# Optimization experiments

Hardware: AMD Instinct MI355X
Metric: run time of the kernel (lower is better)

## Reference

```python
import jax, jax.numpy as jnp
import numpy as np

N_NODES = 50000   # number of graph nodes
N_EDGES = 800000  # avg degree 16
D_IN = 128
D_OUT = 128


def setup_inputs() -> dict:
    key = jax.random.key(0)
    k = jax.random.split(key, 5)
    seq = jax.random.normal(k[0], (N_NODES, D_IN), dtype=jnp.float32)
    # Linear weight, torch layout [out_dim, in_dim], xavier-ish scale
    W = jax.random.normal(k[1], (D_OUT, D_IN), dtype=jnp.float32) * (1.414 / np.sqrt(D_IN))
    b = jnp.zeros((D_OUT,), dtype=jnp.float32)  # bias init fill_(0.0)
    # COO sparse adjacency: out[row] += val * seq_proj[col]
    edge_row = jax.random.randint(k[2], (N_EDGES,), 0, N_NODES, dtype=jnp.int32)
    edge_col = jax.random.randint(k[3], (N_EDGES,), 0, N_NODES, dtype=jnp.int32)
    edge_val = jax.random.uniform(k[4], (N_EDGES,), dtype=jnp.float32)
    return {"seq": seq, "W": W, "b": b,
            "edge_row": edge_row, "edge_col": edge_col, "edge_val": edge_val}


def reference(seq, W, b, edge_row, edge_col, edge_val):
    # seq = self.fc(seq): [N, D_in] @ [D_in, D_out]
    h = seq @ W.T                                   # [N, D_out]
    # out = torch.spmm(adj, h): COO gather-scale-scatter
    msgs = h[edge_col] * edge_val[:, None]          # [E, D_out]
    out = jax.ops.segment_sum(msgs, edge_row, num_segments=N_NODES)  # [N, D_out]
    # bias add + relu (fused epilogue)
    return jax.nn.relu(out + b)
```

## Files before the change

### kernel.cpp

```cpp
#include <hip/hip_runtime.h>

#define NN 50000
#define NE 800000
#define DD 128

#define BK_SHIFT 8
#define NBUCK 196
#define CHUNK 2048
#define NCHUNK 391
#define NGB 782
#define ECAP 8192

#define OFF_H      0
#define OFF_EBIN   3200000
#define OFF_EPACK  6411264
#define OFF_END    8016896
#define OFF_CUR    8066896
#define WS_FULL_FLOATS 8067092

typedef short short8 __attribute__((ext_vector_type(8)));
typedef float f32x4 __attribute__((ext_vector_type(4)));

static __device__ __forceinline__ unsigned int f2bf(float x) {
    unsigned int u = __float_as_uint(x);
    return (u + 0x7fffu + ((u >> 16) & 1u)) >> 16;
}

__global__ __launch_bounds__(256) void k1_scatter_gemm(
        const float* __restrict__ seq, const float* __restrict__ W,
        unsigned short* __restrict__ h,
        const int* __restrict__ erow, const int* __restrict__ ecol,
        const float* __restrict__ eval,
        int* __restrict__ gcur, uint2* __restrict__ ebin) {
    __shared__ uint4 lds4[3072];
    char* lds = (char*)lds4;
    const int t = threadIdx.x;

    if (blockIdx.x < NCHUNK) {
        int* lh = (int*)lds4;
        for (int i = t; i < NBUCK; i += 256) lh[i] = 0;
        __syncthreads();
        const int e0 = blockIdx.x * CHUNK;
        for (int i = t; i < CHUNK; i += 256) {
            int e = e0 + i;
            if (e < NE) atomicAdd(&lh[erow[e] >> BK_SHIFT], 1);
        }
        __syncthreads();
        for (int i = t; i < NBUCK; i += 256) {
            int c = lh[i];
            lh[i] = c ? atomicAdd(&gcur[i], c) : 0;
        }
        __syncthreads();
        for (int i = t; i < CHUNK; i += 256) {
            int e = e0 + i;
            if (e < NE) {
                int r = erow[e], c = ecol[e];
                unsigned int vb = __float_as_uint(eval[e]);
                int k = r >> BK_SHIFT;
                int pos = atomicAdd(&lh[k], 1);
                if (pos < ECAP)
                    ebin[(size_t)k * ECAP + pos] =
                        make_uint2(((unsigned)r << 16) | (unsigned)c, vb);
            }
        }
        return;
    }

    const int base = (blockIdx.x - NCHUNK) * 64;
#define BS_OFF 16384

    {
        const int o = t >> 1, ksb = (t & 1) * 64;
        const float4* Wr = (const float4*)(W + o * 128 + ksb);
#pragma unroll
        for (int i = 0; i < 16; i += 2) {
            float4 x = Wr[i], y = Wr[i + 1];
            uint4 p;
            p.x = f2bf(x.x) | (f2bf(x.y) << 16);
            p.y = f2bf(x.z) | (f2bf(x.w) << 16);
            p.z = f2bf(y.x) | (f2bf(y.y) << 16);
            p.w = f2bf(y.z) | (f2bf(y.w) << 16);
            int byte = o * 256 + (ksb + i * 4) * 2;
            *(uint4*)(lds + BS_OFF + (byte ^ ((o & 7) << 4))) = p;
        }
    }
    {
        const int row = t >> 2, n = base + row;
        const int c0 = (t & 3) * 4;
        const float4* Sr = (const float4*)(seq + (size_t)n * 128);
        const bool ok = (n < NN);
#pragma unroll
        for (int i = 0; i < 4; ++i) {
            int cc = c0 + i;
            float4 x = ok ? Sr[cc * 2]     : make_float4(0.f, 0.f, 0.f, 0.f);
            float4 y = ok ? Sr[cc * 2 + 1] : make_float4(0.f, 0.f, 0.f, 0.f);
            uint4 p;
            p.x = f2bf(x.x) | (f2bf(x.y) << 16);
            p.y = f2bf(x.z) | (f2bf(x.w) << 16);
            p.z = f2bf(y.x) | (f2bf(y.y) << 16);
            p.w = f2bf(y.z) | (f2bf(y.w) << 16);
            int byte = row * 256 + cc * 16;
            *(uint4*)(lds + (byte ^ ((row & 7) << 4))) = p;
        }
    }
    __syncthreads();

    const int l = t & 63, wv = t >> 6;
    const int lr = l & 15, kg = l >> 4;
    const int arow = wv * 16 + lr;
    f32x4 acc[8] = {};

#pragma unroll
    for (int ks = 0; ks < 4; ++ks) {
        const int kbyte = ks * 64 + kg * 16;
        short8 av = *(short8*)(lds + ((arow * 256 + kbyte) ^ ((arow & 7) << 4)));
#pragma unroll
        for (int c = 0; c < 8; ++c) {
            const int o = c * 16 + lr;
            short8 bv = *(short8*)(lds + BS_OFF +
                                   ((o * 256 + kbyte) ^ ((o & 7) << 4)));
            acc[c] = __builtin_amdgcn_mfma_f32_16x16x32_bf16(av, bv, acc[c], 0, 0, 0);
        }
    }

#pragma unroll
    for (int c = 0; c < 8; ++c) {
#pragma unroll
        for (int r = 0; r < 4; ++r) {
            int n = base + wv * 16 + kg * 4 + r;
            if (n < NN)
                h[(size_t)n * DD + c * 16 + lr] = (unsigned short)f2bf(acc[c][r]);
        }
    }
}

__global__ __launch_bounds__(256) void csr_fill(const uint2* __restrict__ ebin,
                                                const int* __restrict__ gcur,
                                                int* __restrict__ endv,
                                                unsigned int* __restrict__ epack) {
    __shared__ int lh[256];
    __shared__ int lx[256];
    const int k = blockIdx.x;
    const int t = threadIdx.x;
    const size_t s0 = (size_t)k * ECAP;
    int cnt = gcur[k];
    if (cnt > ECAP) cnt = ECAP;
    const size_t s1 = s0 + cnt;
    const int r0 = k << BK_SHIFT;

    lh[t] = 0;
    __syncthreads();
    for (size_t e = s0 + t; e < s1; e += 256)
        atomicAdd(&lh[(ebin[e].x >> 16) & 255], 1);
    __syncthreads();

    const int myc = lh[t];
    lx[t] = myc;
    __syncthreads();
    for (int off = 1; off < 256; off <<= 1) {
        int y = (t >= off) ? lx[t - off] : 0;
        __syncthreads();
        lx[t] += y;
        __syncthreads();
    }
    const int incl = lx[t];
    const int row = r0 + t;
    if (row < NN) endv[row] = (int)s0 + incl;
    __syncthreads();
    lh[t] = (int)s0 + incl - myc;
    __syncthreads();

    for (size_t e = s0 + t; e < s1; e += 256) {
        uint2 ed = ebin[e];
        int pos = atomicAdd(&lh[(ed.x >> 16) & 255], 1);
        epack[pos] = (ed.x & 0xffffu) | (f2bf(__uint_as_float(ed.y)) << 16);
    }
}

__global__ __launch_bounds__(256) void gather_kernel(const unsigned short* __restrict__ h,
                                                     const int* __restrict__ end,
                                                     const unsigned int* __restrict__ epack,
                                                     const float* __restrict__ b,
                                                     float* __restrict__ out) {
    const int row  = blockIdx.x * 4 + (threadIdx.x >> 6);
    const int lane = threadIdx.x & 63;
    const int slot = lane >> 4;
    const int sub  = lane & 15;
    const int begin = (row & 255) ? end[row - 1] : (row >> BK_SHIFT) * ECAP;
    const int e1 = end[row];

    float acc[8] = {0.f, 0.f, 0.f, 0.f, 0.f, 0.f, 0.f, 0.f};
    const unsigned short* hp = h + sub * 8;

#define BODY(EE) do {                                                          \
        unsigned int cv = __builtin_nontemporal_load(epack + (EE));            \
        float v = __uint_as_float(cv & 0xffff0000u);                           \
        uint4 hv = *(const uint4*)(hp + (size_t)(cv & 0xffffu) * DD);          \
        unsigned int uu;                                                       \
        uu = hv.x;                                                             \
        acc[0] = fmaf(v, __uint_as_float(uu << 16),          acc[0]);          \
        acc[1] = fmaf(v, __uint_as_float(uu & 0xffff0000u),  acc[1]);          \
        uu = hv.y;                                                             \
        acc[2] = fmaf(v, __uint_as_float(uu << 16),          acc[2]);          \
        acc[3] = fmaf(v, __uint_as_float(uu & 0xffff0000u),  acc[3]);          \
        uu = hv.z;                                                             \
        acc[4] = fmaf(v, __uint_as_float(uu << 16),          acc[4]);          \
        acc[5] = fmaf(v, __uint_as_float(uu & 0xffff0000u),  acc[5]);          \
        uu = hv.w;                                                             \
        acc[6] = fmaf(v, __uint_as_float(uu << 16),          acc[6]);          \
        acc[7] = fmaf(v, __uint_as_float(uu & 0xffff0000u),  acc[7]);          \
    } while (0)

    int e = begin + slot;
    for (; e + 12 < e1; e += 16) { BODY(e); BODY(e + 4); BODY(e + 8); BODY(e + 12); }
    for (; e < e1; e += 4) BODY(e);
#undef BODY

#pragma unroll
    for (int i = 0; i < 8; ++i) {
        acc[i] += __shfl_xor(acc[i], 16);
        acc[i] += __shfl_xor(acc[i], 32);
    }

    if (slot == 0) {
        const float4* b4 = (const float4*)(b + sub * 8);
        float4 b0 = b4[0], b1 = b4[1];
        f32x4 o0, o1;
        o0.x = fmaxf(acc[0] + b0.x, 0.f);
        o0.y = fmaxf(acc[1] + b0.y, 0.f);
        o0.z = fmaxf(acc[2] + b0.z, 0.f);
        o0.w = fmaxf(acc[3] + b0.w, 0.f);
        o1.x = fmaxf(acc[4] + b1.x, 0.f);
        o1.y = fmaxf(acc[5] + b1.y, 0.f);
        o1.z = fmaxf(acc[6] + b1.z, 0.f);
        o1.w = fmaxf(acc[7] + b1.w, 0.f);
        f32x4* op = (f32x4*)(out + (size_t)row * DD + sub * 8);
        __builtin_nontemporal_store(o0, op);
        __builtin_nontemporal_store(o1, op + 1);
    }
}

extern "C" void kernel_launch(void* const* d_in, const int* in_sizes, int n_in,
                              void* d_out, int out_size, void* d_ws, size_t ws_size,
                              hipStream_t stream) {
    const float* seq  = (const float*)d_in[0];
    const float* W    = (const float*)d_in[1];
    const float* b    = (const float*)d_in[2];
    const int*   erow = (const int*)d_in[3];
    const int*   ecol = (const int*)d_in[4];
    const float* eval = (const float*)d_in[5];
    float* out = (float*)d_out;

    float* wsf = (float*)d_ws;
    unsigned short* h  = (unsigned short*)(wsf + OFF_H);
    uint2* ebin  = (uint2*)(wsf + OFF_EBIN);
    unsigned int* epack = (unsigned int*)(wsf + OFF_EPACK);
    int*   endv  = (int*)(wsf + OFF_END);
    int*   gcur  = (int*)(wsf + OFF_CUR);

    hipMemsetAsync(gcur, 0, NBUCK * sizeof(int), stream);
    k1_scatter_gemm<<<NCHUNK + NGB, 256, 0, stream>>>(seq, W, h, erow, ecol,
                                                      eval, gcur, ebin);
    csr_fill<<<NBUCK, 256, 0, stream>>>(ebin, gcur, endv, epack);
    gather_kernel<<<NN / 4, 256, 0, stream>>>(h, endv, epack, b, out);
}
```

Before: 82.91 us.

## Fuse CSR fill into gather kernel with per-bucket LDS edge sorting

Buckets shrink from 256 to 64 rows. The separate csr_fill and gather kernels merge into one kernel: each 512-thread block counting-sorts its bucket's edges into shared memory, then its waves gather rows directly from LDS records. This removes one launch and the global round trip of the packed edge array and the end offsets. The cost is a fixed bucket capacity of 2048 edges, which silently drops overflow edges under skewed inputs, plus only 782 blocks of serialized per-row work.

```diff
diff --git a/kernel.cpp b/kernel.cpp
--- a/kernel.cpp
+++ b/kernel.cpp
@@ -4,19 +4,18 @@
 #define NE 800000
 #define DD 128
 
-#define BK_SHIFT 8
-#define NBUCK 196
-#define CHUNK 2048
-#define NCHUNK 391
+#define BK_SHIFT 6
+#define BROWS 64
+#define NBUCK 782
+#define ECAP 2048
+#define CHUNK 8192
+#define NCHUNK 98
 #define NGB 782
-#define ECAP 8192
 
 #define OFF_H      0
 #define OFF_EBIN   3200000
-#define OFF_EPACK  6411264
-#define OFF_END    8016896
-#define OFF_CUR    8066896
-#define WS_FULL_FLOATS 8067092
+#define OFF_CUR    6403072
+#define WS_FULL_FLOATS 6403854
 
 typedef short short8 __attribute__((ext_vector_type(8)));
 typedef float f32x4 __attribute__((ext_vector_type(4)));
@@ -134,66 +133,55 @@
     }
 }
 
-__global__ __launch_bounds__(256) void csr_fill(const uint2* __restrict__ ebin,
-                                                const int* __restrict__ gcur,
-                                                int* __restrict__ endv,
-                                                unsigned int* __restrict__ epack) {
-    __shared__ int lh[256];
-    __shared__ int lx[256];
-    const int k = blockIdx.x;
-    const int t = threadIdx.x;
-    const size_t s0 = (size_t)k * ECAP;
+__global__ __launch_bounds__(512) void k2_fill_gather(
+        const unsigned short* __restrict__ h,
+        const uint2* __restrict__ ebin,
+        const int* __restrict__ gcur,
+        const float* __restrict__ bias,
+        float* __restrict__ out) {
+    __shared__ unsigned int recs[ECAP];
+    __shared__ int lh[BROWS];
+    __shared__ int rend[BROWS];
+    __shared__ int rcur[BROWS];
+    const int k = blockIdx.x, t = threadIdx.x;
+    const int wid = t >> 6, lane = t & 63;
+
     int cnt = gcur[k];
     if (cnt > ECAP) cnt = ECAP;
-    const size_t s1 = s0 + cnt;
-    const int r0 = k << BK_SHIFT;
-
-    lh[t] = 0;
-    __syncthreads();
-    for (size_t e = s0 + t; e < s1; e += 256)
-        atomicAdd(&lh[(ebin[e].x >> 16) & 255], 1);
-    __syncthreads();
-
-    const int myc = lh[t];
-    lx[t] = myc;
-    __syncthreads();
-    for (int off = 1; off < 256; off <<= 1) {
-        int y = (t >= off) ? lx[t - off] : 0;
-        __syncthreads();
-        lx[t] += y;
-        __syncthreads();
-    }
-    const int incl = lx[t];
-    const int row = r0 + t;
-    if (row < NN) endv[row] = (int)s0 + incl;
-    __syncthreads();
-    lh[t] = (int)s0 + incl - myc;
-    __syncthreads();
-
-    for (size_t e = s0 + t; e < s1; e += 256) {
-        uint2 ed = ebin[e];
-        int pos = atomicAdd(&lh[(ed.x >> 16) & 255], 1);
-        epack[pos] = (ed.x & 0xffffu) | (f2bf(__uint_as_float(ed.y)) << 16);
-    }
-}
-
-__global__ __launch_bounds__(256) void gather_kernel(const unsigned short* __restrict__ h,
-                                                     const int* __restrict__ end,
-                                                     const unsigned int* __restrict__ epack,
-                                                     const float* __restrict__ b,
-                                                     float* __restrict__ out) {
-    const int row  = blockIdx.x * 4 + (threadIdx.x >> 6);
-    const int lane = threadIdx.x & 63;
+    const uint2* eb = ebin + (size_t)k * ECAP;
+
+    if (t < BROWS) lh[t] = 0;
+    __syncthreads();
+    for (int e = t; e < cnt; e += 512)
+        atomicAdd(&lh[(eb[e].x >> 16) & (BROWS - 1)], 1);
+    __syncthreads();
+    if (t < BROWS) {
+        int x = lh[t];
+#pragma unroll
+        for (int off = 1; off < 64; off <<= 1) {
+            int y = __shfl_up(x, off);
+            if (lane >= off) x += y;
+        }
+        rend[t] = x;
+        rcur[t] = x - lh[t];
+    }
+    __syncthreads();
+    for (int e = t; e < cnt; e += 512) {
+        uint2 ed = eb[e];
+        int row = (ed.x >> 16) & (BROWS - 1);
+        int pos = atomicAdd(&rcur[row], 1);
+        recs[pos] = (ed.x & 0xffffu) | (f2bf(__uint_as_float(ed.y)) << 16);
+    }
+    __syncthreads();
+
     const int slot = lane >> 4;
     const int sub  = lane & 15;
-    const int begin = (row & 255) ? end[row - 1] : (row >> BK_SHIFT) * ECAP;
-    const int e1 = end[row];
-
-    float acc[8] = {0.f, 0.f, 0.f, 0.f, 0.f, 0.f, 0.f, 0.f};
     const unsigned short* hp = h + sub * 8;
+    const float4* b4 = (const float4*)(bias + sub * 8);
+    const float4 b0 = b4[0], b1 = b4[1];
 
 #define BODY(EE) do {                                                          \
-        unsigned int cv = __builtin_nontemporal_load(epack + (EE));            \
+        unsigned int cv = recs[EE];                                            \
         float v = __uint_as_float(cv & 0xffff0000u);                           \
         uint4 hv = *(const uint4*)(hp + (size_t)(cv & 0xffffu) * DD);          \
         unsigned int uu;                                                       \
@@ -211,33 +199,42 @@
         acc[7] = fmaf(v, __uint_as_float(uu & 0xffff0000u),  acc[7]);          \
     } while (0)
 
-    int e = begin + slot;
-    for (; e + 12 < e1; e += 16) { BODY(e); BODY(e + 4); BODY(e + 8); BODY(e + 12); }
-    for (; e < e1; e += 4) BODY(e);
+#pragma unroll 1
+    for (int ri = 0; ri < 8; ++ri) {
+        const int row = wid * 8 + ri;
+        const int begin = row ? rend[row - 1] : 0;
+        const int e1 = rend[row];
+        float acc[8] = {0.f, 0.f, 0.f, 0.f, 0.f, 0.f, 0.f, 0.f};
+
+        int e = begin + slot;
+        for (; e + 12 < e1; e += 16) { BODY(e); BODY(e + 4); BODY(e + 8); BODY(e + 12); }
+        for (; e < e1; e += 4) BODY(e);
+
+#pragma unroll
+        for (int i = 0; i < 8; ++i) {
+            acc[i] += __shfl_xor(acc[i], 16);
+            acc[i] += __shfl_xor(acc[i], 32);
+        }
+
+        if (slot == 0) {
+            const int n = (k << BK_SHIFT) + row;
+            if (n < NN) {
+                f32x4 o0, o1;
+                o0.x = fmaxf(acc[0] + b0.x, 0.f);
+                o0.y = fmaxf(acc[1] + b0.y, 0.f);
+                o0.z = fmaxf(acc[2] + b0.z, 0.f);
+                o0.w = fmaxf(acc[3] + b0.w, 0.f);
+                o1.x = fmaxf(acc[4] + b1.x, 0.f);
+                o1.y = fmaxf(acc[5] + b1.y, 0.f);
+                o1.z = fmaxf(acc[6] + b1.z, 0.f);
+                o1.w = fmaxf(acc[7] + b1.w, 0.f);
+                f32x4* op = (f32x4*)(out + (size_t)n * DD + sub * 8);
+                __builtin_nontemporal_store(o0, op);
+                __builtin_nontemporal_store(o1, op + 1);
+            }
+        }
+    }
 #undef BODY
-
-#pragma unroll
-    for (int i = 0; i < 8; ++i) {
-        acc[i] += __shfl_xor(acc[i], 16);
-        acc[i] += __shfl_xor(acc[i], 32);
-    }
-
-    if (slot == 0) {
-        const float4* b4 = (const float4*)(b + sub * 8);
-        float4 b0 = b4[0], b1 = b4[1];
-        f32x4 o0, o1;
-        o0.x = fmaxf(acc[0] + b0.x, 0.f);
-        o0.y = fmaxf(acc[1] + b0.y, 0.f);
-        o0.z = fmaxf(acc[2] + b0.z, 0.f);
-        o0.w = fmaxf(acc[3] + b0.w, 0.f);
-        o1.x = fmaxf(acc[4] + b1.x, 0.f);
-        o1.y = fmaxf(acc[5] + b1.y, 0.f);
-        o1.z = fmaxf(acc[6] + b1.z, 0.f);
-        o1.w = fmaxf(acc[7] + b1.w, 0.f);
-        f32x4* op = (f32x4*)(out + (size_t)row * DD + sub * 8);
-        __builtin_nontemporal_store(o0, op);
-        __builtin_nontemporal_store(o1, op + 1);
-    }
 }
 
 extern "C" void kernel_launch(void* const* d_in, const int* in_sizes, int n_in,
@@ -252,15 +249,12 @@
     float* out = (float*)d_out;
 
     float* wsf = (float*)d_ws;
-    unsigned short* h  = (unsigned short*)(wsf + OFF_H);
-    uint2* ebin  = (uint2*)(wsf + OFF_EBIN);
-    unsigned int* epack = (unsigned int*)(wsf + OFF_EPACK);
-    int*   endv  = (int*)(wsf + OFF_END);
-    int*   gcur  = (int*)(wsf + OFF_CUR);
+    unsigned short* h = (unsigned short*)(wsf + OFF_H);
+    uint2* ebin = (uint2*)(wsf + OFF_EBIN);
+    int*   gcur = (int*)(wsf + OFF_CUR);
 
     hipMemsetAsync(gcur, 0, NBUCK * sizeof(int), stream);
     k1_scatter_gemm<<<NCHUNK + NGB, 256, 0, stream>>>(seq, W, h, erow, ecol,
                                                       eval, gcur, ebin);
-    csr_fill<<<NBUCK, 256, 0, stream>>>(ebin, gcur, endv, epack);
-    gather_kernel<<<NN / 4, 256, 0, stream>>>(h, endv, epack, b, out);
-}
+    k2_fill_gather<<<NBUCK, 512, 0, stream>>>(h, ebin, gcur, b, out);
+}
```

Measured after the change: 84.88 us. 1.02x slower.
